# Kernel tuning notes

Hardware: AMD Instinct MI355X
Metric: run time of the kernel (lower is better)

## Reference

```python
import jax, jax.numpy as jnp
import numpy as np

B, D, N = 256, 256, 100000
NUM_CLUSTERS, NUM_CLASSES = 100, 1000


def setup_inputs() -> dict:
    key = jax.random.key(0)
    k1, k2, k3, k4, k5, k6 = jax.random.split(key, 6)
    return {
        "feature": jax.random.normal(k1, (B, D), dtype=jnp.float32),
        "feature_bank": jax.random.normal(k2, (N, D), dtype=jnp.float32),
        "cluster_label_bank": jax.random.randint(k3, (N,), 0, NUM_CLUSTERS, dtype=jnp.int64)
            if jax.config.jax_enable_x64 else jax.random.randint(k3, (N,), 0, NUM_CLUSTERS).astype(jnp.int32),
        "class_label_bank": jax.random.randint(k4, (N,), 0, NUM_CLASSES).astype(jnp.int32),
        "cluster_idx": jax.random.randint(k5, (B,), 0, NUM_CLUSTERS).astype(jnp.int32),
        "gt_label": jax.random.randint(k6, (B,), 0, NUM_CLASSES).astype(jnp.int32),
    }


def reference(feature, feature_bank, cluster_label_bank, class_label_bank, cluster_idx, gt_label):
    # Masks: primary = same cluster AND different class; fallback = different class only.
    cluster_label_bank = cluster_label_bank.astype(jnp.int32)
    same_cluster = cluster_label_bank[None, :] == cluster_idx[:, None].astype(jnp.int32)  # [B, N]
    diff_class = class_label_bank[None, :] != gt_label[:, None]                            # [B, N]
    mask_primary = same_cluster & diff_class
    has_primary = mask_primary.any(axis=1, keepdims=True)
    mask = jnp.where(has_primary, mask_primary, diff_class)  # [B, N]

    # Euclidean distances (torch.cdist p=2): ||a-b|| via expanded squared form.
    a2 = jnp.sum(feature * feature, axis=1)[:, None]              # [B, 1]
    b2 = jnp.sum(feature_bank * feature_bank, axis=1)[None, :]    # [1, N]
    d2 = a2 + b2 - 2.0 * (feature @ feature_bank.T)               # [B, N]
    dist = jnp.sqrt(jnp.maximum(d2, 0.0))

    # Masked argmin over the bank, then gather negatives.
    dist_masked = jnp.where(mask, dist, jnp.inf)
    neg_idx = jnp.argmin(dist_masked, axis=1)                     # [B]
    negatives = feature_bank[neg_idx]                             # [B, D]
    return negatives
```

## Files before the change

kernel.cpp:

```cpp
#include <hip/hip_runtime.h>
#include <climits>

typedef __attribute__((ext_vector_type(8))) short s8;
typedef __attribute__((ext_vector_type(4))) float f32x4;

#define BQ    256
#define DDIM  256
#define NBANK 100000
#define BN    64
#define NJB   ((NBANK + BN - 1) / BN)
#define SENT  1e30f

__device__ inline void splitElem(float x, s8& h, s8& l, int i) {
    unsigned u  = __float_as_uint(x);
    unsigned uh = (u + 0x8000u) & 0xFFFF0000u;
    h[i] = (short)(uh >> 16);
    float lf = x - __uint_as_float(uh);
    l[i] = (short)((__float_as_uint(lf) + 0x8000u) >> 16);
}

__device__ inline void split8(const float4 v0, const float4 v1, s8& h, s8& l) {
    splitElem(v0.x, h, l, 0); splitElem(v0.y, h, l, 1);
    splitElem(v0.z, h, l, 2); splitElem(v0.w, h, l, 3);
    splitElem(v1.x, h, l, 4); splitElem(v1.y, h, l, 5);
    splitElem(v1.z, h, l, 6); splitElem(v1.w, h, l, 7);
}

__device__ inline float sq8(const float4 v0, const float4 v1, float s) {
    s = fmaf(v0.x, v0.x, s); s = fmaf(v0.y, v0.y, s);
    s = fmaf(v0.z, v0.z, s); s = fmaf(v0.w, v0.w, s);
    s = fmaf(v1.x, v1.x, s); s = fmaf(v1.y, v1.y, s);
    s = fmaf(v1.z, v1.z, s); s = fmaf(v1.w, v1.w, s);
    return s;
}

__global__ __launch_bounds__(512) void split_feature(
    const float* __restrict__ feature, s8* __restrict__ fH, s8* __restrict__ fL)
{
    const int t    = blockIdx.x * 512 + threadIdx.x;
    const int lane = t & 63, ks = (t >> 6) & 7, rt = t >> 9;
    const int row  = rt * 16 + (lane & 15);
    const int k0   = ks * 32 + (lane >> 4) * 8;
    const float* p = feature + (size_t)row * DDIM + k0;
    const float4 v0 = *(const float4*)p;
    const float4 v1 = *(const float4*)(p + 4);
    s8 h, l;
    split8(v0, v1, h, l);
    fH[t] = h; fL[t] = l;
}

__global__ __launch_bounds__(512, 4) void gemm_argmin_fullk(
    const s8* __restrict__ fH, const s8* __restrict__ fL,
    const float* __restrict__ bank,
    const int* __restrict__ cluster_label, const int* __restrict__ class_label,
    const int* __restrict__ cluster_idx,  const int* __restrict__ gt_label,
    float* __restrict__ wsPV, int* __restrict__ wsPI,
    float* __restrict__ wsDV, int* __restrict__ wsDI)
{
    __shared__ __align__(16) s8 bHs[8 * 4 * 64];
    __shared__ __align__(16) s8 bLs[8 * 4 * 64];
    __shared__ float b2s[BN];
    __shared__ int clsS[BN], cluS[BN], rowGt[BQ], rowClu[BQ];

    const int tid = threadIdx.x;
    const int jb  = blockIdx.x;
    const int j0  = jb * BN;

    if (tid < BN) {
        int jg = j0 + tid;
        int jc = jg < NBANK ? jg : NBANK - 1;
        clsS[tid] = class_label[jc];
        cluS[tid] = cluster_label[jc];
    }
    if (tid < BQ) {
        rowGt[tid]  = gt_label[tid];
        rowClu[tid] = cluster_idx[tid];
    }

    const int col = tid >> 3, q = tid & 7;
    const int ct_s = col >> 4, cl_s = col & 15;
    int jcol = j0 + col; jcol = jcol < NBANK ? jcol : NBANK - 1;
    const float* gb = bank + (size_t)jcol * DDIM + q * 32;

    float4 v0[4], v1[4];
    #pragma unroll
    for (int i = 0; i < 4; ++i) {
        v0[i] = *(const float4*)(gb + i * 8);
        v1[i] = *(const float4*)(gb + i * 8 + 4);
    }
    float sqa = 0.f;
    #pragma unroll
    for (int i = 0; i < 4; ++i) {
        s8 h, l;
        split8(v0[i], v1[i], h, l);
        sqa = sq8(v0[i], v1[i], sqa);
        const int wi = (q * 4 + ct_s) * 64 + i * 16 + cl_s;
        bHs[wi] = h;
        bLs[wi] = l;
    }
    sqa += __shfl_xor(sqa, 1);
    sqa += __shfl_xor(sqa, 2);
    sqa += __shfl_xor(sqa, 4);
    if (q == 0) b2s[col] = sqa;
    __syncthreads();

    const int w = tid >> 6, lane = tid & 63;
    const int g = lane >> 4, c = lane & 15;

    f32x4 acc[4][2];
    #pragma unroll
    for (int ct = 0; ct < 4; ++ct)
        #pragma unroll
        for (int rt = 0; rt < 2; ++rt)
            acc[ct][rt] = (f32x4){0.f, 0.f, 0.f, 0.f};

    #pragma unroll
    for (int s = 0; s < 8; ++s) {
        s8 aH[2], aL[2];
        #pragma unroll
        for (int rt = 0; rt < 2; ++rt) {
            const int RT = w * 2 + rt;
            aH[rt] = fH[(RT * 8 + s) * 64 + lane];
            aL[rt] = fL[(RT * 8 + s) * 64 + lane];
        }
        #pragma unroll
        for (int ct = 0; ct < 4; ++ct) {
            const s8 bh = bHs[(s * 4 + ct) * 64 + lane];
            const s8 bl = bLs[(s * 4 + ct) * 64 + lane];
            #pragma unroll
            for (int rt = 0; rt < 2; ++rt) {
                acc[ct][rt] = __builtin_amdgcn_mfma_f32_16x16x32_bf16(aH[rt], bh, acc[ct][rt], 0, 0, 0);
                acc[ct][rt] = __builtin_amdgcn_mfma_f32_16x16x32_bf16(aH[rt], bl, acc[ct][rt], 0, 0, 0);
                acc[ct][rt] = __builtin_amdgcn_mfma_f32_16x16x32_bf16(aL[rt], bh, acc[ct][rt], 0, 0, 0);
                acc[ct][rt] = __builtin_amdgcn_mfma_f32_16x16x32_bf16(aL[rt], bl, acc[ct][rt], 0, 0, 0);
            }
        }
    }

    #pragma unroll
    for (int rt = 0; rt < 2; ++rt) {
        #pragma unroll
        for (int r = 0; r < 4; ++r) {
            const int row  = w * 32 + rt * 16 + g * 4 + r;
            const int myGt = rowGt[row], myClu = rowClu[row];
            float bpv = SENT, bdv = SENT;
            int   bpi = INT_MAX, bdi = INT_MAX;
            #pragma unroll
            for (int ct = 0; ct < 4; ++ct) {
                const int jg = j0 + ct * 16 + c;
                const float sc = b2s[ct * 16 + c] - 2.f * acc[ct][rt][r];
                if (jg < NBANK && clsS[ct * 16 + c] != myGt) {
                    if (sc < bdv) { bdv = sc; bdi = jg; }
                    if (cluS[ct * 16 + c] == myClu && sc < bpv) { bpv = sc; bpi = jg; }
                }
            }
            #pragma unroll
            for (int off = 1; off < 16; off <<= 1) {
                float vv = __shfl_xor(bpv, off); int ii = __shfl_xor(bpi, off);
                if (vv < bpv || (vv == bpv && ii < bpi)) { bpv = vv; bpi = ii; }
                vv = __shfl_xor(bdv, off); ii = __shfl_xor(bdi, off);
                if (vv < bdv || (vv == bdv && ii < bdi)) { bdv = vv; bdi = ii; }
            }
            if (c == 0) {
                const size_t o = (size_t)jb * BQ + row;
                wsPV[o] = bpv; wsPI[o] = bpi;
                wsDV[o] = bdv; wsDI[o] = bdi;
            }
        }
    }
}

__global__ __launch_bounds__(256) void reduce_gather(
    const float* __restrict__ wsPV, const int* __restrict__ wsPI,
    const float* __restrict__ wsDV, const int* __restrict__ wsDI,
    const float* __restrict__ bank, float* __restrict__ out)
{
    const int row = blockIdx.x, tid = threadIdx.x;
    float bpv = SENT, bdv = SENT;
    int   bpi = INT_MAX, bdi = INT_MAX;
    for (int b = tid; b < NJB; b += 256) {
        const size_t o = (size_t)b * BQ + row;
        float v = wsPV[o]; int ix = wsPI[o];
        if (v < bpv || (v == bpv && ix < bpi)) { bpv = v; bpi = ix; }
        v = wsDV[o]; ix = wsDI[o];
        if (v < bdv || (v == bdv && ix < bdi)) { bdv = v; bdi = ix; }
    }
    #pragma unroll
    for (int off = 32; off > 0; off >>= 1) {
        float v = __shfl_down(bpv, off); int ix = __shfl_down(bpi, off);
        if (v < bpv || (v == bpv && ix < bpi)) { bpv = v; bpi = ix; }
        v = __shfl_down(bdv, off); ix = __shfl_down(bdi, off);
        if (v < bdv || (v == bdv && ix < bdi)) { bdv = v; bdi = ix; }
    }
    __shared__ float swPV[4], swDV[4];
    __shared__ int   swPI[4], swDI[4];
    __shared__ int   sIdx;
    const int lane = tid & 63, wv = tid >> 6;
    if (lane == 0) { swPV[wv] = bpv; swPI[wv] = bpi; swDV[wv] = bdv; swDI[wv] = bdi; }
    __syncthreads();
    if (tid == 0) {
        float pv = swPV[0]; int pi = swPI[0];
        float dv = swDV[0]; int di = swDI[0];
        #pragma unroll
        for (int w = 1; w < 4; ++w) {
            if (swPV[w] < pv || (swPV[w] == pv && swPI[w] < pi)) { pv = swPV[w]; pi = swPI[w]; }
            if (swDV[w] < dv || (swDV[w] == dv && swDI[w] < di)) { dv = swDV[w]; di = swDI[w]; }
        }
        sIdx = (pi != INT_MAX) ? pi : ((di != INT_MAX) ? di : 0);
    }
    __syncthreads();
    out[row * DDIM + tid] = bank[(size_t)sIdx * DDIM + tid];
}

extern "C" void kernel_launch(void* const* d_in, const int* in_sizes, int n_in,
                              void* d_out, int out_size, void* d_ws, size_t ws_size,
                              hipStream_t stream) {
    const float* feature       = (const float*)d_in[0];
    const float* bank          = (const float*)d_in[1];
    const int*   cluster_label = (const int*)d_in[2];
    const int*   class_label   = (const int*)d_in[3];
    const int*   cluster_idx   = (const int*)d_in[4];
    const int*   gt_label      = (const int*)d_in[5];
    float* out = (float*)d_out;

    s8* fH = (s8*)d_ws;
    s8* fL = fH + 8192;
    float* base = (float*)((char*)d_ws + 2 * 8192 * sizeof(s8));
    const size_t per = (size_t)BQ * NJB;
    float* wsPV = base;
    int*   wsPI = (int*)base + per;
    float* wsDV = base + 2 * per;
    int*   wsDI = (int*)base + 3 * per;

    hipLaunchKernelGGL(split_feature, dim3(16), dim3(512), 0, stream, feature, fH, fL);
    hipLaunchKernelGGL(gemm_argmin_fullk, dim3(NJB), dim3(512), 0, stream,
                       fH, fL, bank, cluster_label, class_label, cluster_idx, gt_label,
                       wsPV, wsPI, wsDV, wsDI);
    hipLaunchKernelGGL(reduce_gather, dim3(BQ), dim3(256), 0, stream,
                       wsPV, wsPI, wsDV, wsDI, bank, out);
}
```

Baseline: 241.0 us.

## Make GEMM-argmin kernel persistent with prefetch of next bank tile

Replaces the one-block-per-tile grid with a persistent grid of 512 blocks that loop over bank tiles. Each iteration prefetches the next tile's bank rows and labels into registers while the current tile's MFMA work runs, hiding global load latency. It also XOR-swizzles the LDS indices for the split bank tiles to reduce bank conflicts. In exchange it adds an extra barrier per iteration and more register pressure from holding the prefetched data, which could cut occupancy.

```diff
diff --git a/kernel.cpp b/kernel.cpp
--- a/kernel.cpp
+++ b/kernel.cpp
@@ -9,6 +9,7 @@
 #define NBANK 100000
 #define BN    64
 #define NJB   ((NBANK + BN - 1) / BN)
+#define GRIDX 512
 #define SENT  1e30f
 
 __device__ inline void splitElem(float x, s8& h, s8& l, int i) {
@@ -49,7 +50,7 @@
     fH[t] = h; fL[t] = l;
 }
 
-__global__ __launch_bounds__(512, 4) void gemm_argmin_fullk(
+__global__ __launch_bounds__(512, 4) void gemm_argmin_persist(
     const s8* __restrict__ fH, const s8* __restrict__ fL,
     const float* __restrict__ bank,
     const int* __restrict__ cluster_label, const int* __restrict__ class_label,
@@ -63,15 +64,6 @@
     __shared__ int clsS[BN], cluS[BN], rowGt[BQ], rowClu[BQ];
 
     const int tid = threadIdx.x;
-    const int jb  = blockIdx.x;
-    const int j0  = jb * BN;
-
-    if (tid < BN) {
-        int jg = j0 + tid;
-        int jc = jg < NBANK ? jg : NBANK - 1;
-        clsS[tid] = class_label[jc];
-        cluS[tid] = cluster_label[jc];
-    }
     if (tid < BQ) {
         rowGt[tid]  = gt_label[tid];
         rowClu[tid] = cluster_idx[tid];
@@ -79,94 +71,129 @@
 
     const int col = tid >> 3, q = tid & 7;
     const int ct_s = col >> 4, cl_s = col & 15;
-    int jcol = j0 + col; jcol = jcol < NBANK ? jcol : NBANK - 1;
-    const float* gb = bank + (size_t)jcol * DDIM + q * 32;
-
-    float4 v0[4], v1[4];
-    #pragma unroll
-    for (int i = 0; i < 4; ++i) {
-        v0[i] = *(const float4*)(gb + i * 8);
-        v1[i] = *(const float4*)(gb + i * 8 + 4);
-    }
-    float sqa = 0.f;
-    #pragma unroll
-    for (int i = 0; i < 4; ++i) {
-        s8 h, l;
-        split8(v0[i], v1[i], h, l);
-        sqa = sq8(v0[i], v1[i], sqa);
-        const int wi = (q * 4 + ct_s) * 64 + i * 16 + cl_s;
-        bHs[wi] = h;
-        bLs[wi] = l;
-    }
-    sqa += __shfl_xor(sqa, 1);
-    sqa += __shfl_xor(sqa, 2);
-    sqa += __shfl_xor(sqa, 4);
-    if (q == 0) b2s[col] = sqa;
-    __syncthreads();
-
     const int w = tid >> 6, lane = tid & 63;
     const int g = lane >> 4, c = lane & 15;
 
-    f32x4 acc[4][2];
-    #pragma unroll
-    for (int ct = 0; ct < 4; ++ct)
-        #pragma unroll
-        for (int rt = 0; rt < 2; ++rt)
-            acc[ct][rt] = (f32x4){0.f, 0.f, 0.f, 0.f};
-
-    #pragma unroll
-    for (int s = 0; s < 8; ++s) {
-        s8 aH[2], aL[2];
+    int jb = blockIdx.x;
+
+    float4 v0[4], v1[4];
+    int lblC = 0, lblU = 0;
+    {
+        int jcol = jb * BN + col; if (jcol >= NBANK) jcol = NBANK - 1;
+        const float* gb = bank + (size_t)jcol * DDIM + q * 32;
+        #pragma unroll
+        for (int i = 0; i < 4; ++i) {
+            v0[i] = *(const float4*)(gb + i * 8);
+            v1[i] = *(const float4*)(gb + i * 8 + 4);
+        }
+        if (tid < BN) {
+            int jg = jb * BN + tid; int jc = jg < NBANK ? jg : NBANK - 1;
+            lblC = class_label[jc];
+            lblU = cluster_label[jc];
+        }
+    }
+
+    for (;;) {
+        const int j0 = jb * BN;
+
+        float sqa = 0.f;
+        #pragma unroll
+        for (int i = 0; i < 4; ++i) {
+            s8 h, l;
+            split8(v0[i], v1[i], h, l);
+            sqa = sq8(v0[i], v1[i], sqa);
+            const int wi = ((q * 4 + ct_s) * 64 + i * 16 + cl_s) ^ q;
+            bHs[wi] = h;
+            bLs[wi] = l;
+        }
+        sqa += __shfl_xor(sqa, 1);
+        sqa += __shfl_xor(sqa, 2);
+        sqa += __shfl_xor(sqa, 4);
+        if (q == 0) b2s[col] = sqa;
+        if (tid < BN) { clsS[tid] = lblC; cluS[tid] = lblU; }
+        __syncthreads();
+
+        const int jbn = jb + GRIDX;
+        const bool more = (jbn < NJB);
+        if (more) {
+            int jcol = jbn * BN + col; if (jcol >= NBANK) jcol = NBANK - 1;
+            const float* gb = bank + (size_t)jcol * DDIM + q * 32;
+            #pragma unroll
+            for (int i = 0; i < 4; ++i) {
+                v0[i] = *(const float4*)(gb + i * 8);
+                v1[i] = *(const float4*)(gb + i * 8 + 4);
+            }
+            if (tid < BN) {
+                int jg = jbn * BN + tid; int jc = jg < NBANK ? jg : NBANK - 1;
+                lblC = class_label[jc];
+                lblU = cluster_label[jc];
+            }
+        }
+
+        f32x4 acc[4][2];
+        #pragma unroll
+        for (int ct = 0; ct < 4; ++ct)
+            #pragma unroll
+            for (int rt = 0; rt < 2; ++rt)
+                acc[ct][rt] = (f32x4){0.f, 0.f, 0.f, 0.f};
+
+        #pragma unroll
+        for (int s = 0; s < 8; ++s) {
+            s8 aH[2], aL[2];
+            #pragma unroll
+            for (int rt = 0; rt < 2; ++rt) {
+                const int RT = w * 2 + rt;
+                aH[rt] = fH[(RT * 8 + s) * 64 + lane];
+                aL[rt] = fL[(RT * 8 + s) * 64 + lane];
+            }
+            #pragma unroll
+            for (int ct = 0; ct < 4; ++ct) {
+                const s8 bh = bHs[((s * 4 + ct) * 64 + lane) ^ s];
+                const s8 bl = bLs[((s * 4 + ct) * 64 + lane) ^ s];
+                #pragma unroll
+                for (int rt = 0; rt < 2; ++rt) {
+                    acc[ct][rt] = __builtin_amdgcn_mfma_f32_16x16x32_bf16(aH[rt], bh, acc[ct][rt], 0, 0, 0);
+                    acc[ct][rt] = __builtin_amdgcn_mfma_f32_16x16x32_bf16(aH[rt], bl, acc[ct][rt], 0, 0, 0);
+                    acc[ct][rt] = __builtin_amdgcn_mfma_f32_16x16x32_bf16(aL[rt], bh, acc[ct][rt], 0, 0, 0);
+                    acc[ct][rt] = __builtin_amdgcn_mfma_f32_16x16x32_bf16(aL[rt], bl, acc[ct][rt], 0, 0, 0);
+                }
+            }
+        }
+
         #pragma unroll
         for (int rt = 0; rt < 2; ++rt) {
-            const int RT = w * 2 + rt;
-            aH[rt] = fH[(RT * 8 + s) * 64 + lane];
-            aL[rt] = fL[(RT * 8 + s) * 64 + lane];
-        }
-        #pragma unroll
-        for (int ct = 0; ct < 4; ++ct) {
-            const s8 bh = bHs[(s * 4 + ct) * 64 + lane];
-            const s8 bl = bLs[(s * 4 + ct) * 64 + lane];
-            #pragma unroll
-            for (int rt = 0; rt < 2; ++rt) {
-                acc[ct][rt] = __builtin_amdgcn_mfma_f32_16x16x32_bf16(aH[rt], bh, acc[ct][rt], 0, 0, 0);
-                acc[ct][rt] = __builtin_amdgcn_mfma_f32_16x16x32_bf16(aH[rt], bl, acc[ct][rt], 0, 0, 0);
-                acc[ct][rt] = __builtin_amdgcn_mfma_f32_16x16x32_bf16(aL[rt], bh, acc[ct][rt], 0, 0, 0);
-                acc[ct][rt] = __builtin_amdgcn_mfma_f32_16x16x32_bf16(aL[rt], bl, acc[ct][rt], 0, 0, 0);
-            }
-        }
-    }
-
-    #pragma unroll
-    for (int rt = 0; rt < 2; ++rt) {
-        #pragma unroll
-        for (int r = 0; r < 4; ++r) {
-            const int row  = w * 32 + rt * 16 + g * 4 + r;
-            const int myGt = rowGt[row], myClu = rowClu[row];
-            float bpv = SENT, bdv = SENT;
-            int   bpi = INT_MAX, bdi = INT_MAX;
-            #pragma unroll
-            for (int ct = 0; ct < 4; ++ct) {
-                const int jg = j0 + ct * 16 + c;
-                const float sc = b2s[ct * 16 + c] - 2.f * acc[ct][rt][r];
-                if (jg < NBANK && clsS[ct * 16 + c] != myGt) {
-                    if (sc < bdv) { bdv = sc; bdi = jg; }
-                    if (cluS[ct * 16 + c] == myClu && sc < bpv) { bpv = sc; bpi = jg; }
-                }
-            }
-            #pragma unroll
-            for (int off = 1; off < 16; off <<= 1) {
-                float vv = __shfl_xor(bpv, off); int ii = __shfl_xor(bpi, off);
-                if (vv < bpv || (vv == bpv && ii < bpi)) { bpv = vv; bpi = ii; }
-                vv = __shfl_xor(bdv, off); ii = __shfl_xor(bdi, off);
-                if (vv < bdv || (vv == bdv && ii < bdi)) { bdv = vv; bdi = ii; }
-            }
-            if (c == 0) {
-                const size_t o = (size_t)jb * BQ + row;
-                wsPV[o] = bpv; wsPI[o] = bpi;
-                wsDV[o] = bdv; wsDI[o] = bdi;
-            }
-        }
+            #pragma unroll
+            for (int r = 0; r < 4; ++r) {
+                const int row  = w * 32 + rt * 16 + g * 4 + r;
+                const int myGt = rowGt[row], myClu = rowClu[row];
+                float bpv = SENT, bdv = SENT;
+                int   bpi = INT_MAX, bdi = INT_MAX;
+                #pragma unroll
+                for (int ct = 0; ct < 4; ++ct) {
+                    const int jg = j0 + ct * 16 + c;
+                    const float sc = b2s[ct * 16 + c] - 2.f * acc[ct][rt][r];
+                    if (jg < NBANK && clsS[ct * 16 + c] != myGt) {
+                        if (sc < bdv) { bdv = sc; bdi = jg; }
+                        if (cluS[ct * 16 + c] == myClu && sc < bpv) { bpv = sc; bpi = jg; }
+                    }
+                }
+                #pragma unroll
+                for (int off = 1; off < 16; off <<= 1) {
+                    float vv = __shfl_xor(bpv, off); int ii = __shfl_xor(bpi, off);
+                    if (vv < bpv || (vv == bpv && ii < bpi)) { bpv = vv; bpi = ii; }
+                    vv = __shfl_xor(bdv, off); ii = __shfl_xor(bdi, off);
+                    if (vv < bdv || (vv == bdv && ii < bdi)) { bdv = vv; bdi = ii; }
+                }
+                if (c == 0) {
+                    const size_t o = (size_t)jb * BQ + row;
+                    wsPV[o] = bpv; wsPI[o] = bpi;
+                    wsDV[o] = bdv; wsDI[o] = bdi;
+                }
+            }
+        }
+        __syncthreads();
+        if (!more) break;
+        jb = jbn;
     }
 }
 
@@ -233,7 +260,7 @@
     int*   wsDI = (int*)base + 3 * per;
 
     hipLaunchKernelGGL(split_feature, dim3(16), dim3(512), 0, stream, feature, fH, fL);
-    hipLaunchKernelGGL(gemm_argmin_fullk, dim3(NJB), dim3(512), 0, stream,
+    hipLaunchKernelGGL(gemm_argmin_persist, dim3(GRIDX), dim3(512), 0, stream,
                        fH, fL, bank, cluster_label, class_label, cluster_idx, gt_label,
                        wsPV, wsPI, wsDV, wsDI);
     hipLaunchKernelGGL(reduce_gather, dim3(BQ), dim3(256), 0, stream,
```

After: 300.7 us. +24.8%, slower.

## Split bank tile K-dimension into two halves with prefetch and swizzled LDS

Applied to the files above, without the earlier changes.

The GEMM-argmin kernel now stages the bank tile in two K-halves, halving the shared-memory buffers. The second half's global loads are issued before the first half's MFMA loop, so memory latency overlaps compute. LDS writes and reads use an XOR swizzle to reduce bank conflicts, and launch bounds now target 8 blocks per CU for higher occupancy. The cost is an extra barrier and a second split pass, plus register pressure from the prefetched values under the tighter launch bound.

```diff
diff --git a/kernel.cpp b/kernel.cpp
--- a/kernel.cpp
+++ b/kernel.cpp
@@ -49,7 +49,7 @@
     fH[t] = h; fL[t] = l;
 }
 
-__global__ __launch_bounds__(512, 4) void gemm_argmin_fullk(
+__global__ __launch_bounds__(512, 8) void gemm_argmin_halfk(
     const s8* __restrict__ fH, const s8* __restrict__ fL,
     const float* __restrict__ bank,
     const int* __restrict__ cluster_label, const int* __restrict__ class_label,
@@ -57,8 +57,8 @@
     float* __restrict__ wsPV, int* __restrict__ wsPI,
     float* __restrict__ wsDV, int* __restrict__ wsDI)
 {
-    __shared__ __align__(16) s8 bHs[8 * 4 * 64];
-    __shared__ __align__(16) s8 bLs[8 * 4 * 64];
+    __shared__ __align__(16) s8 bHs[4 * 4 * 64];
+    __shared__ __align__(16) s8 bLs[4 * 4 * 64];
     __shared__ float b2s[BN];
     __shared__ int clsS[BN], cluS[BN], rowGt[BQ], rowClu[BQ];
 
@@ -66,37 +66,90 @@
     const int jb  = blockIdx.x;
     const int j0  = jb * BN;
 
-    if (tid < BN) {
-        int jg = j0 + tid;
-        int jc = jg < NBANK ? jg : NBANK - 1;
-        clsS[tid] = class_label[jc];
-        cluS[tid] = cluster_label[jc];
-    }
+    const int col = tid >> 3, q = tid & 7;
+    const int ct_s = col >> 4, cl_s = col & 15;
+    const int sl_s = q >> 1, p_s = q & 1;
+    const int w = tid >> 6, lane = tid & 63;
+    const int g = lane >> 4, c = lane & 15;
+
+    int jcol = j0 + col; if (jcol >= NBANK) jcol = NBANK - 1;
+    const float* gb = bank + (size_t)jcol * DDIM + q * 16;
+
     if (tid < BQ) {
         rowGt[tid]  = gt_label[tid];
         rowClu[tid] = cluster_idx[tid];
     }
-
-    const int col = tid >> 3, q = tid & 7;
-    const int ct_s = col >> 4, cl_s = col & 15;
-    int jcol = j0 + col; jcol = jcol < NBANK ? jcol : NBANK - 1;
-    const float* gb = bank + (size_t)jcol * DDIM + q * 32;
-
-    float4 v0[4], v1[4];
-    #pragma unroll
-    for (int i = 0; i < 4; ++i) {
-        v0[i] = *(const float4*)(gb + i * 8);
-        v1[i] = *(const float4*)(gb + i * 8 + 4);
-    }
+    if (tid < BN) {
+        int jg = j0 + tid; int jc = jg < NBANK ? jg : NBANK - 1;
+        clsS[tid] = class_label[jc];
+        cluS[tid] = cluster_label[jc];
+    }
+    float4 a0 = *(const float4*)(gb);
+    float4 a1 = *(const float4*)(gb + 4);
+    float4 a2 = *(const float4*)(gb + 8);
+    float4 a3 = *(const float4*)(gb + 12);
+
     float sqa = 0.f;
-    #pragma unroll
-    for (int i = 0; i < 4; ++i) {
+    {
         s8 h, l;
-        split8(v0[i], v1[i], h, l);
-        sqa = sq8(v0[i], v1[i], sqa);
-        const int wi = (q * 4 + ct_s) * 64 + i * 16 + cl_s;
-        bHs[wi] = h;
-        bLs[wi] = l;
+        split8(a0, a1, h, l);
+        sqa = sq8(a0, a1, sqa);
+        int wi = (((sl_s * 4 + ct_s) * 64 + (p_s * 2 + 0) * 16 + cl_s)) ^ q;
+        bHs[wi] = h; bLs[wi] = l;
+        split8(a2, a3, h, l);
+        sqa = sq8(a2, a3, sqa);
+        wi = (((sl_s * 4 + ct_s) * 64 + (p_s * 2 + 1) * 16 + cl_s)) ^ q;
+        bHs[wi] = h; bLs[wi] = l;
+    }
+    __syncthreads();
+
+    a0 = *(const float4*)(gb + 128);
+    a1 = *(const float4*)(gb + 132);
+    a2 = *(const float4*)(gb + 136);
+    a3 = *(const float4*)(gb + 140);
+
+    f32x4 acc[4][2];
+    #pragma unroll
+    for (int ct = 0; ct < 4; ++ct)
+        #pragma unroll
+        for (int rt = 0; rt < 2; ++rt)
+            acc[ct][rt] = (f32x4){0.f, 0.f, 0.f, 0.f};
+
+    #pragma unroll
+    for (int sl = 0; sl < 4; ++sl) {
+        s8 aH[2], aL[2];
+        #pragma unroll
+        for (int rt = 0; rt < 2; ++rt) {
+            const int RT = w * 2 + rt;
+            aH[rt] = fH[(RT * 8 + sl) * 64 + lane];
+            aL[rt] = fL[(RT * 8 + sl) * 64 + lane];
+        }
+        const int rx = sl * 2 + (lane >> 5);
+        #pragma unroll
+        for (int ct = 0; ct < 4; ++ct) {
+            const s8 bh = bHs[((sl * 4 + ct) * 64 + lane) ^ rx];
+            const s8 bl = bLs[((sl * 4 + ct) * 64 + lane) ^ rx];
+            #pragma unroll
+            for (int rt = 0; rt < 2; ++rt) {
+                acc[ct][rt] = __builtin_amdgcn_mfma_f32_16x16x32_bf16(aH[rt], bh, acc[ct][rt], 0, 0, 0);
+                acc[ct][rt] = __builtin_amdgcn_mfma_f32_16x16x32_bf16(aH[rt], bl, acc[ct][rt], 0, 0, 0);
+                acc[ct][rt] = __builtin_amdgcn_mfma_f32_16x16x32_bf16(aL[rt], bh, acc[ct][rt], 0, 0, 0);
+                acc[ct][rt] = __builtin_amdgcn_mfma_f32_16x16x32_bf16(aL[rt], bl, acc[ct][rt], 0, 0, 0);
+            }
+        }
+    }
+    __syncthreads();
+
+    {
+        s8 h, l;
+        split8(a0, a1, h, l);
+        sqa = sq8(a0, a1, sqa);
+        int wi = (((sl_s * 4 + ct_s) * 64 + (p_s * 2 + 0) * 16 + cl_s)) ^ q;
+        bHs[wi] = h; bLs[wi] = l;
+        split8(a2, a3, h, l);
+        sqa = sq8(a2, a3, sqa);
+        wi = (((sl_s * 4 + ct_s) * 64 + (p_s * 2 + 1) * 16 + cl_s)) ^ q;
+        bHs[wi] = h; bLs[wi] = l;
     }
     sqa += __shfl_xor(sqa, 1);
     sqa += __shfl_xor(sqa, 2);
@@ -104,29 +157,20 @@
     if (q == 0) b2s[col] = sqa;
     __syncthreads();
 
-    const int w = tid >> 6, lane = tid & 63;
-    const int g = lane >> 4, c = lane & 15;
-
-    f32x4 acc[4][2];
-    #pragma unroll
-    for (int ct = 0; ct < 4; ++ct)
-        #pragma unroll
-        for (int rt = 0; rt < 2; ++rt)
-            acc[ct][rt] = (f32x4){0.f, 0.f, 0.f, 0.f};
-
-    #pragma unroll
-    for (int s = 0; s < 8; ++s) {
+    #pragma unroll
+    for (int sl = 0; sl < 4; ++sl) {
         s8 aH[2], aL[2];
         #pragma unroll
         for (int rt = 0; rt < 2; ++rt) {
             const int RT = w * 2 + rt;
-            aH[rt] = fH[(RT * 8 + s) * 64 + lane];
-            aL[rt] = fL[(RT * 8 + s) * 64 + lane];
-        }
+            aH[rt] = fH[(RT * 8 + 4 + sl) * 64 + lane];
+            aL[rt] = fL[(RT * 8 + 4 + sl) * 64 + lane];
+        }
+        const int rx = sl * 2 + (lane >> 5);
         #pragma unroll
         for (int ct = 0; ct < 4; ++ct) {
-            const s8 bh = bHs[(s * 4 + ct) * 64 + lane];
-            const s8 bl = bLs[(s * 4 + ct) * 64 + lane];
+            const s8 bh = bHs[((sl * 4 + ct) * 64 + lane) ^ rx];
+            const s8 bl = bLs[((sl * 4 + ct) * 64 + lane) ^ rx];
             #pragma unroll
             for (int rt = 0; rt < 2; ++rt) {
                 acc[ct][rt] = __builtin_amdgcn_mfma_f32_16x16x32_bf16(aH[rt], bh, acc[ct][rt], 0, 0, 0);
@@ -233,7 +277,7 @@
     int*   wsDI = (int*)base + 3 * per;
 
     hipLaunchKernelGGL(split_feature, dim3(16), dim3(512), 0, stream, feature, fH, fL);
-    hipLaunchKernelGGL(gemm_argmin_fullk, dim3(NJB), dim3(512), 0, stream,
+    hipLaunchKernelGGL(gemm_argmin_halfk, dim3(NJB), dim3(512), 0, stream,
                        fH, fL, bank, cluster_label, class_label, cluster_idx, gt_label,
                        wsPV, wsPI, wsDV, wsDI);
     hipLaunchKernelGGL(reduce_gather, dim3(BQ), dim3(256), 0, stream,
```

New measurement: 289.1 us. 1.2x slower.
